# Kernel optimization log

Hardware: AMD Instinct MI355X
Metric: run time of the kernel (lower is better)

## Reference

```python
import jax, jax.numpy as jnp
import numpy as np

B, T, E, DH = 4, 4096, 1024, 128

def setup_inputs() -> dict:
    key = jax.random.key(0)
    k1, k2, k3, k4 = jax.random.split(key, 4)
    scale = 1.0 / np.sqrt(E)
    return {
        "norm_inputs": jax.random.normal(k1, (B, T, E), dtype=jnp.float32),
        "Wq": jax.random.normal(k2, (E, DH), dtype=jnp.float32) * scale,
        "Wk": jax.random.normal(k3, (E, DH), dtype=jnp.float32) * scale,
        "Wv": jax.random.normal(k4, (E, DH), dtype=jnp.float32) * scale,
    }

def reference(norm_inputs, Wq, Wk, Wv):
    # q,k,v: [B,T,DH]
    q = jnp.einsum("bte,ed->btd", norm_inputs, Wq)
    k = jnp.einsum("bte,ed->btd", norm_inputs, Wk)
    v = jnp.einsum("bte,ed->btd", norm_inputs, Wv)
    Tn = norm_inputs.shape[1]
    # scaled scores [B,T,T]
    scores = jnp.einsum("bqd,bkd->bqk", q, k) / jnp.sqrt(jnp.asarray(q.shape[-1], q.dtype))
    causal = jnp.tril(jnp.ones((Tn, Tn), dtype=bool))
    scores = jnp.where(causal, scores, -jnp.inf)
    attn = jax.nn.softmax(scores, axis=-1)  # dropout p=0 -> identity
    return jnp.einsum("bqk,bkd->bqd", attn, v)
```

## Files before the change

### kernel.cpp

```cpp
#include <hip/hip_runtime.h>
#include <hip/hip_bf16.h>

#define NB 4
#define NT 4096
#define NE 1024
#define ND 128
#define QSCALE 0.12751741f

typedef unsigned u32x4 __attribute__((ext_vector_type(4)));
typedef float f32x4 __attribute__((ext_vector_type(4)));
typedef float f32x16 __attribute__((ext_vector_type(16)));
typedef __bf16 bf16x8 __attribute__((ext_vector_type(8)));
typedef unsigned short u16;

__device__ __forceinline__ unsigned cvt_pk_bf16(float lo, float hi) {
  unsigned r;
  asm("v_cvt_pk_bf16_f32 %0, %1, %2" : "=v"(r) : "v"(lo), "v"(hi));
  return r;
}
__device__ __forceinline__ void permswap(unsigned& a, unsigned& b) {
  asm("v_permlane32_swap_b32 %0, %1" : "+v"(a), "+v"(b));
}
__device__ __forceinline__ u16 f2bf(float f) {
  unsigned x = __float_as_uint(f);
  x += 0x7fffu + ((x >> 16) & 1u);
  return (u16)(x >> 16);
}
__device__ __forceinline__ f32x16 mfma32(bf16x8 a, bf16x8 b, f32x16 c) {
  return __builtin_amdgcn_mfma_f32_32x32x16_bf16(a, b, c, 0, 0, 0);
}
__device__ __forceinline__ bf16x8 ldb(const u16* p) {
  return *reinterpret_cast<const bf16x8*>(p);
}
__device__ __forceinline__ void pack_pf(const f32x16& pr, bf16x8& f0, bf16x8& f1) {
  unsigned pk[8];
#pragma unroll
  for (int i = 0; i < 8; ++i) pk[i] = cvt_pk_bf16(pr[2 * i], pr[2 * i + 1]);
  permswap(pk[0], pk[2]);
  permswap(pk[1], pk[3]);
  permswap(pk[4], pk[6]);
  permswap(pk[5], pk[7]);
  u32x4 t0, t1;
  t0[0] = pk[0]; t0[1] = pk[1]; t0[2] = pk[2]; t0[3] = pk[3];
  t1[0] = pk[4]; t1[1] = pk[5]; t1[2] = pk[6]; t1[3] = pk[7];
  f0 = __builtin_bit_cast(bf16x8, t0);
  f1 = __builtin_bit_cast(bf16x8, t1);
}

__global__ void ah_prep(const float* __restrict__ Wq, const float* __restrict__ Wk,
                        const float* __restrict__ Wv, u16* __restrict__ wt) {
  const int m = blockIdx.x >> 5;
  const int r = blockIdx.x & 31;
  const int e0 = (r >> 1) * 64;
  const int d0 = (r & 1) * 64;
  const float* W = (m == 0) ? Wq : (m == 1) ? Wk : Wv;
  const float s = (m == 0) ? QSCALE : 1.0f;
  __shared__ u16 lds[64][68];
  const int t = threadIdx.x;
  const int row = t >> 2;
  const int c0 = (t & 3) * 16;
  const float* src = W + (size_t)(e0 + row) * ND + d0 + c0;
#pragma unroll
  for (int i = 0; i < 16; i += 4) {
    f32x4 v = *reinterpret_cast<const f32x4*>(src + i);
#pragma unroll
    for (int j = 0; j < 4; ++j) lds[c0 + i + j][row] = f2bf(v[j] * s);
  }
  __syncthreads();
  const int d = t >> 2;
  const int ec = (t & 3) * 16;
  u16* dst = wt + (size_t)m * NE * ND + (size_t)(d0 + d) * NE + e0 + ec;
  u32x4 o0, o1;
#pragma unroll
  for (int j = 0; j < 4; ++j)
    o0[j] = (unsigned)lds[d][ec + 2 * j] | ((unsigned)lds[d][ec + 2 * j + 1] << 16);
#pragma unroll
  for (int j = 0; j < 4; ++j)
    o1[j] = (unsigned)lds[d][ec + 8 + 2 * j] | ((unsigned)lds[d][ec + 8 + 2 * j + 1] << 16);
  *reinterpret_cast<u32x4*>(dst) = o0;
  *reinterpret_cast<u32x4*>(dst + 8) = o1;
}

__global__ __launch_bounds__(256, 2) void ah_proj(
    const float* __restrict__ X, const u16* __restrict__ wt,
    u16* __restrict__ qb, u16* __restrict__ kb, u16* __restrict__ vtb) {
  const int row0 = blockIdx.x * 32;
  const int tid = threadIdx.x;
  const int w = tid >> 6;
  const int lane = tid & 63;
  const int l31 = lane & 31;
  const int h = lane >> 5;

  const float* xrow = X + (size_t)(row0 + l31) * NE + h * 8;
  const u16* wpQ = wt + (size_t)(w * 32 + l31) * NE + h * 8;
  const u16* wpK = wpQ + (size_t)NE * ND;
  const u16* wpV = wpK + (size_t)NE * ND;

  f32x16 accQ = {}, accK = {}, accV = {};

#pragma unroll 2
  for (int e0 = 0; e0 < NE; e0 += 16) {
    f32x4 x0 = *reinterpret_cast<const f32x4*>(xrow + e0);
    f32x4 x1 = *reinterpret_cast<const f32x4*>(xrow + e0 + 4);
    u32x4 xw;
    xw[0] = cvt_pk_bf16(x0[0], x0[1]);
    xw[1] = cvt_pk_bf16(x0[2], x0[3]);
    xw[2] = cvt_pk_bf16(x1[0], x1[1]);
    xw[3] = cvt_pk_bf16(x1[2], x1[3]);
    bf16x8 xf = __builtin_bit_cast(bf16x8, xw);
    accQ = mfma32(xf, ldb(wpQ + e0), accQ);
    accK = mfma32(xf, ldb(wpK + e0), accK);
    accV = mfma32(ldb(wpV + e0), xf, accV);
  }

  const int col = w * 32 + l31;
#pragma unroll
  for (int r = 0; r < 16; ++r) {
    const int trow = row0 + (r & 3) + 8 * (r >> 2) + 4 * h;
    qb[(size_t)trow * ND + col] = f2bf(accQ[r]);
    kb[(size_t)trow * ND + col] = f2bf(accK[r]);
  }
  const int bb = row0 >> 12;
  const int tt = (row0 & 4095) + l31;
#pragma unroll
  for (int r = 0; r < 16; ++r) {
    const int d = w * 32 + (r & 3) + 8 * (r >> 2) + 4 * h;
    vtb[(size_t)bb * ND * NT + (size_t)d * NT + tt] = f2bf(accV[r]);
  }
}

__global__ __launch_bounds__(256, 2) void ah_attn(
    const u16* __restrict__ qg, const u16* __restrict__ kg,
    const u16* __restrict__ vtg, float* __restrict__ out) {
  __shared__ float smem_m[4][32];
  __shared__ float smem_l[4][32];
  __shared__ float smem_linv[32];
  __shared__ float smemO[128][33];

  const int bid = blockIdx.x;
  const int xcd = bid & 7;
  const int slot = bid >> 3;
  const int b = xcd >> 1;
  const int qt = 127 - (slot * 2 + (xcd & 1));
  const int q0 = qt * 32;
  const int tid = threadIdx.x;
  const int w = tid >> 6;
  const int lane = tid & 63;
  const int l31 = lane & 31;
  const int h = lane >> 5;

  const u16* Qb = qg + (size_t)b * NT * ND;
  const u16* Kb = kg + (size_t)b * NT * ND;
  const u16* VTb = vtg + (size_t)b * ND * NT;
  float* Ob = out + (size_t)b * NT * ND;

  bf16x8 qf[8];
  {
    const u16* qrow = Qb + (size_t)(q0 + l31) * ND + h * 8;
#pragma unroll
    for (int s = 0; s < 8; ++s) qf[s] = ldb(qrow + s * 16);
  }

  float m_run = -1e30f, l_run = 0.f;
  f32x16 ot[4] = {};

  const int ntiles = qt + 1;
  for (int j0 = w; j0 < ntiles; j0 += 8) {
    const int j1 = j0 + 4;
    const bool has1 = (j1 < ntiles);
    const int k0 = j0 * 32;
    const int k1 = has1 ? j1 * 32 : k0;
    f32x16 sa = {}, sb = {};
    const u16* krow0 = Kb + (size_t)(k0 + l31) * ND + h * 8;
    const u16* krow1 = Kb + (size_t)(k1 + l31) * ND + h * 8;
#pragma unroll
    for (int s = 0; s < 8; ++s) {
      sa = mfma32(ldb(krow0 + s * 16), qf[s], sa);
      sb = mfma32(ldb(krow1 + s * 16), qf[s], sb);
    }
    if (j0 == qt) {
#pragma unroll
      for (int r = 0; r < 16; ++r) {
        const int kk = (r & 3) + 8 * (r >> 2) + 4 * h;
        if (kk > l31) sa[r] = -1e30f;
      }
    }
    if (has1) {
      if (j1 == qt) {
#pragma unroll
        for (int r = 0; r < 16; ++r) {
          const int kk = (r & 3) + 8 * (r >> 2) + 4 * h;
          if (kk > l31) sb[r] = -1e30f;
        }
      }
    } else {
#pragma unroll
      for (int r = 0; r < 16; ++r) sb[r] = -1e30f;
    }
    float mt = sa[0];
#pragma unroll
    for (int r = 1; r < 16; ++r) mt = fmaxf(mt, sa[r]);
#pragma unroll
    for (int r = 0; r < 16; ++r) mt = fmaxf(mt, sb[r]);
    mt = fmaxf(mt, __shfl_xor(mt, 32));
    if (__any(mt > m_run + 8.f)) {
      const float mn = fmaxf(m_run, mt);
      const float f = __builtin_amdgcn_exp2f(m_run - mn);
      l_run *= f;
#pragma unroll
      for (int d0 = 0; d0 < 4; ++d0) ot[d0] *= f;
      m_run = mn;
    }
    float ps = 0.f;
#pragma unroll
    for (int r = 0; r < 16; ++r) {
      sa[r] = __builtin_amdgcn_exp2f(sa[r] - m_run);
      ps += sa[r];
    }
#pragma unroll
    for (int r = 0; r < 16; ++r) {
      sb[r] = __builtin_amdgcn_exp2f(sb[r] - m_run);
      ps += sb[r];
    }
    ps += __shfl_xor(ps, 32);
    l_run += ps;
    bf16x8 pf0a, pf0b, pf1a, pf1b;
    pack_pf(sa, pf0a, pf0b);
    pack_pf(sb, pf1a, pf1b);
#pragma unroll
    for (int d0 = 0; d0 < 4; ++d0) {
      const u16* vrow0 = VTb + (size_t)(d0 * 32 + l31) * NT + k0 + h * 8;
      const u16* vrow1 = VTb + (size_t)(d0 * 32 + l31) * NT + k1 + h * 8;
      ot[d0] = mfma32(ldb(vrow0), pf0a, ot[d0]);
      ot[d0] = mfma32(ldb(vrow0 + 16), pf0b, ot[d0]);
      ot[d0] = mfma32(ldb(vrow1), pf1a, ot[d0]);
      ot[d0] = mfma32(ldb(vrow1 + 16), pf1b, ot[d0]);
    }
  }

  if (h == 0) { smem_m[w][l31] = m_run; smem_l[w][l31] = l_run; }
  __syncthreads();
  float mstar = smem_m[0][l31];
#pragma unroll
  for (int wv = 1; wv < 4; ++wv) mstar = fmaxf(mstar, smem_m[wv][l31]);
  float lstar = 0.f;
#pragma unroll
  for (int wv = 0; wv < 4; ++wv)
    lstar += smem_l[wv][l31] * __builtin_amdgcn_exp2f(smem_m[wv][l31] - mstar);
  if (tid < 32) smem_linv[tid] = 1.0f / lstar;
  const float fw = __builtin_amdgcn_exp2f(m_run - mstar);
  for (int rnd = 0; rnd < 4; ++rnd) {
    if (w == rnd) {
#pragma unroll
      for (int d0 = 0; d0 < 4; ++d0)
#pragma unroll
        for (int r = 0; r < 16; ++r) {
          const int d = d0 * 32 + (r & 3) + 8 * (r >> 2) + 4 * h;
          const float v = ot[d0][r] * fw;
          if (rnd == 0) smemO[d][l31] = v;
          else smemO[d][l31] += v;
        }
    }
    __syncthreads();
  }
  {
    const int q = tid >> 3;
    const int dbase = (tid & 7) * 16;
    const float linv = smem_linv[q];
    float* orow = Ob + (size_t)(q0 + q) * ND + dbase;
#pragma unroll
    for (int c = 0; c < 4; ++c) {
      f32x4 v4;
#pragma unroll
      for (int e = 0; e < 4; ++e) v4[e] = smemO[dbase + c * 4 + e][q] * linv;
      *reinterpret_cast<f32x4*>(orow + c * 4) = v4;
    }
  }
}

extern "C" void kernel_launch(void* const* d_in, const int* in_sizes, int n_in,
                              void* d_out, int out_size, void* d_ws, size_t ws_size,
                              hipStream_t stream) {
  const float* X = (const float*)d_in[0];
  const float* Wq = (const float*)d_in[1];
  const float* Wk = (const float*)d_in[2];
  const float* Wv = (const float*)d_in[3];
  u16* ws = (u16*)d_ws;
  u16* wt = ws;
  u16* qb = wt + 393216;
  u16* kb = qb + 2097152;
  u16* vtb = kb + 2097152;
  float* out = (float*)d_out;

  ah_prep<<<96, 256, 0, stream>>>(Wq, Wk, Wv, wt);
  ah_proj<<<512, 256, 0, stream>>>(X, wt, qb, kb, vtb);
  ah_attn<<<512, 256, 0, stream>>>(qb, kb, vtb, out);
}
```

Before: 265.2 us.

## Split causal attention along the key axis into chunks and add a combine kernel

```diff
diff --git a/kernel.cpp b/kernel.cpp
--- a/kernel.cpp
+++ b/kernel.cpp
@@ -25,6 +25,9 @@
   unsigned x = __float_as_uint(f);
   x += 0x7fffu + ((x >> 16) & 1u);
   return (u16)(x >> 16);
+}
+__device__ __forceinline__ float bf2f(u16 u) {
+  return __uint_as_float(((unsigned)u) << 16);
 }
 __device__ __forceinline__ f32x16 mfma32(bf16x8 a, bf16x8 b, f32x16 c) {
   return __builtin_amdgcn_mfma_f32_32x32x16_bf16(a, b, c, 0, 0, 0);
@@ -98,7 +101,7 @@
 
   f32x16 accQ = {}, accK = {}, accV = {};
 
-#pragma unroll 2
+#pragma unroll 4
   for (int e0 = 0; e0 < NE; e0 += 16) {
     f32x4 x0 = *reinterpret_cast<const f32x4*>(xrow + e0);
     f32x4 x1 = *reinterpret_cast<const f32x4*>(xrow + e0 + 4);
@@ -129,20 +132,29 @@
   }
 }
 
-__global__ __launch_bounds__(256, 2) void ah_attn(
+__global__ __launch_bounds__(256, 4) void ah_attn_sk(
     const u16* __restrict__ qg, const u16* __restrict__ kg,
-    const u16* __restrict__ vtg, float* __restrict__ out) {
+    const u16* __restrict__ vtg, u16* __restrict__ opart,
+    float* __restrict__ ml) {
   __shared__ float smem_m[4][32];
   __shared__ float smem_l[4][32];
-  __shared__ float smem_linv[32];
   __shared__ float smemO[128][33];
 
   const int bid = blockIdx.x;
-  const int xcd = bid & 7;
-  const int slot = bid >> 3;
-  const int b = xcd >> 1;
-  const int qt = 127 - (slot * 2 + (xcd & 1));
+  const int x = bid & 7;
+  const int s = bid >> 3;
+  const int b = x >> 1;
+  const int p = x & 1;
+  int r, c;
+  if (s < 64)       { r = s >> 2;               c = s & 3; }
+  else if (s < 112) { int t = s - 64; int q3 = t / 3; r = 16 + q3; c = t - 3 * q3; }
+  else if (s < 144) { int t = s - 112; r = 32 + (t >> 1); c = t & 1; }
+  else              { r = 48 + (s - 144);       c = 0; }
+  const int qt = (126 + p) - 2 * r;
   const int q0 = qt * 32;
+  const int jbeg = c * 32;
+  const int jend = min(jbeg + 32, qt + 1);
+
   const int tid = threadIdx.x;
   const int w = tid >> 6;
   const int lane = tid & 63;
@@ -152,56 +164,54 @@
   const u16* Qb = qg + (size_t)b * NT * ND;
   const u16* Kb = kg + (size_t)b * NT * ND;
   const u16* VTb = vtg + (size_t)b * ND * NT;
-  float* Ob = out + (size_t)b * NT * ND;
 
   bf16x8 qf[8];
   {
     const u16* qrow = Qb + (size_t)(q0 + l31) * ND + h * 8;
 #pragma unroll
-    for (int s = 0; s < 8; ++s) qf[s] = ldb(qrow + s * 16);
+    for (int sI = 0; sI < 8; ++sI) qf[sI] = ldb(qrow + sI * 16);
   }
 
   float m_run = -1e30f, l_run = 0.f;
   f32x16 ot[4] = {};
 
-  const int ntiles = qt + 1;
-  for (int j0 = w; j0 < ntiles; j0 += 8) {
+  for (int j0 = jbeg + w; j0 < jend; j0 += 8) {
     const int j1 = j0 + 4;
-    const bool has1 = (j1 < ntiles);
+    const bool has1 = (j1 < jend);
     const int k0 = j0 * 32;
     const int k1 = has1 ? j1 * 32 : k0;
     f32x16 sa = {}, sb = {};
     const u16* krow0 = Kb + (size_t)(k0 + l31) * ND + h * 8;
     const u16* krow1 = Kb + (size_t)(k1 + l31) * ND + h * 8;
 #pragma unroll
-    for (int s = 0; s < 8; ++s) {
-      sa = mfma32(ldb(krow0 + s * 16), qf[s], sa);
-      sb = mfma32(ldb(krow1 + s * 16), qf[s], sb);
+    for (int sI = 0; sI < 8; ++sI) {
+      sa = mfma32(ldb(krow0 + sI * 16), qf[sI], sa);
+      sb = mfma32(ldb(krow1 + sI * 16), qf[sI], sb);
     }
     if (j0 == qt) {
 #pragma unroll
-      for (int r = 0; r < 16; ++r) {
-        const int kk = (r & 3) + 8 * (r >> 2) + 4 * h;
-        if (kk > l31) sa[r] = -1e30f;
+      for (int r2 = 0; r2 < 16; ++r2) {
+        const int kk = (r2 & 3) + 8 * (r2 >> 2) + 4 * h;
+        if (kk > l31) sa[r2] = -1e30f;
       }
     }
     if (has1) {
       if (j1 == qt) {
 #pragma unroll
-        for (int r = 0; r < 16; ++r) {
-          const int kk = (r & 3) + 8 * (r >> 2) + 4 * h;
-          if (kk > l31) sb[r] = -1e30f;
+        for (int r2 = 0; r2 < 16; ++r2) {
+          const int kk = (r2 & 3) + 8 * (r2 >> 2) + 4 * h;
+          if (kk > l31) sb[r2] = -1e30f;
         }
       }
     } else {
 #pragma unroll
-      for (int r = 0; r < 16; ++r) sb[r] = -1e30f;
+      for (int r2 = 0; r2 < 16; ++r2) sb[r2] = -1e30f;
     }
     float mt = sa[0];
 #pragma unroll
-    for (int r = 1; r < 16; ++r) mt = fmaxf(mt, sa[r]);
-#pragma unroll
-    for (int r = 0; r < 16; ++r) mt = fmaxf(mt, sb[r]);
+    for (int r2 = 1; r2 < 16; ++r2) mt = fmaxf(mt, sa[r2]);
+#pragma unroll
+    for (int r2 = 0; r2 < 16; ++r2) mt = fmaxf(mt, sb[r2]);
     mt = fmaxf(mt, __shfl_xor(mt, 32));
     if (__any(mt > m_run + 8.f)) {
       const float mn = fmaxf(m_run, mt);
@@ -213,14 +223,14 @@
     }
     float ps = 0.f;
 #pragma unroll
-    for (int r = 0; r < 16; ++r) {
-      sa[r] = __builtin_amdgcn_exp2f(sa[r] - m_run);
-      ps += sa[r];
-    }
-#pragma unroll
-    for (int r = 0; r < 16; ++r) {
-      sb[r] = __builtin_amdgcn_exp2f(sb[r] - m_run);
-      ps += sb[r];
+    for (int r2 = 0; r2 < 16; ++r2) {
+      sa[r2] = __builtin_amdgcn_exp2f(sa[r2] - m_run);
+      ps += sa[r2];
+    }
+#pragma unroll
+    for (int r2 = 0; r2 < 16; ++r2) {
+      sb[r2] = __builtin_amdgcn_exp2f(sb[r2] - m_run);
+      ps += sb[r2];
     }
     ps += __shfl_xor(ps, 32);
     l_run += ps;
@@ -247,34 +257,101 @@
 #pragma unroll
   for (int wv = 0; wv < 4; ++wv)
     lstar += smem_l[wv][l31] * __builtin_amdgcn_exp2f(smem_m[wv][l31] - mstar);
-  if (tid < 32) smem_linv[tid] = 1.0f / lstar;
   const float fw = __builtin_amdgcn_exp2f(m_run - mstar);
   for (int rnd = 0; rnd < 4; ++rnd) {
     if (w == rnd) {
 #pragma unroll
       for (int d0 = 0; d0 < 4; ++d0)
 #pragma unroll
-        for (int r = 0; r < 16; ++r) {
-          const int d = d0 * 32 + (r & 3) + 8 * (r >> 2) + 4 * h;
-          const float v = ot[d0][r] * fw;
+        for (int r2 = 0; r2 < 16; ++r2) {
+          const int d = d0 * 32 + (r2 & 3) + 8 * (r2 >> 2) + 4 * h;
+          const float v = ot[d0][r2] * fw;
           if (rnd == 0) smemO[d][l31] = v;
           else smemO[d][l31] += v;
         }
     }
     __syncthreads();
   }
+  const int slot = ((b * 128 + qt) << 2) + c;
+  if (tid < 32) {
+    ml[(size_t)slot * 64 + tid] = mstar;
+    ml[(size_t)slot * 64 + 32 + tid] = lstar;
+  }
   {
     const int q = tid >> 3;
     const int dbase = (tid & 7) * 16;
-    const float linv = smem_linv[q];
-    float* orow = Ob + (size_t)(q0 + q) * ND + dbase;
-#pragma unroll
-    for (int c = 0; c < 4; ++c) {
-      f32x4 v4;
-#pragma unroll
-      for (int e = 0; e < 4; ++e) v4[e] = smemO[dbase + c * 4 + e][q] * linv;
-      *reinterpret_cast<f32x4*>(orow + c * 4) = v4;
-    }
+    u32x4 o0, o1;
+#pragma unroll
+    for (int k = 0; k < 4; ++k)
+      o0[k] = cvt_pk_bf16(smemO[dbase + 2 * k][q], smemO[dbase + 2 * k + 1][q]);
+#pragma unroll
+    for (int k = 0; k < 4; ++k)
+      o1[k] = cvt_pk_bf16(smemO[dbase + 8 + 2 * k][q], smemO[dbase + 9 + 2 * k][q]);
+    u16* dst = opart + (size_t)slot * 4096 + q * ND + dbase;
+    *reinterpret_cast<u32x4*>(dst) = o0;
+    *reinterpret_cast<u32x4*>(dst + 8) = o1;
+  }
+}
+
+__global__ __launch_bounds__(256, 4) void ah_comb(
+    const u16* __restrict__ opart, const float* __restrict__ ml,
+    float* __restrict__ out) {
+  const int bid = blockIdx.x;
+  const int x = bid & 7;
+  const int r = bid >> 3;
+  const int b = x >> 1;
+  const int p = x & 1;
+  const int qt = (126 + p) - 2 * r;
+  const int q0 = qt * 32;
+  const int nch = (qt + 32) >> 5;
+  const int slot0 = (b * 128 + qt) << 2;
+
+  const int tid = threadIdx.x;
+  const int q = tid >> 3;
+  const int dbase = (tid & 7) * 16;
+
+  float mi0 = -1e30f, mi1 = -1e30f, mi2 = -1e30f, mi3 = -1e30f;
+  mi0 = ml[(size_t)slot0 * 64 + q];
+  if (nch > 1) mi1 = ml[(size_t)(slot0 + 1) * 64 + q];
+  if (nch > 2) mi2 = ml[(size_t)(slot0 + 2) * 64 + q];
+  if (nch > 3) mi3 = ml[(size_t)(slot0 + 3) * 64 + q];
+  const float M = fmaxf(fmaxf(mi0, mi1), fmaxf(mi2, mi3));
+  float sc0 = __builtin_amdgcn_exp2f(mi0 - M);
+  float sc1 = __builtin_amdgcn_exp2f(mi1 - M);
+  float sc2 = __builtin_amdgcn_exp2f(mi2 - M);
+  float sc3 = __builtin_amdgcn_exp2f(mi3 - M);
+  float L = ml[(size_t)slot0 * 64 + 32 + q] * sc0;
+  if (nch > 1) L += ml[(size_t)(slot0 + 1) * 64 + 32 + q] * sc1;
+  if (nch > 2) L += ml[(size_t)(slot0 + 2) * 64 + 32 + q] * sc2;
+  if (nch > 3) L += ml[(size_t)(slot0 + 3) * 64 + 32 + q] * sc3;
+
+  float acc[16];
+#pragma unroll
+  for (int k = 0; k < 16; ++k) acc[k] = 0.f;
+#pragma unroll
+  for (int i = 0; i < 4; ++i) {
+    if (i < nch) {
+      const float sc = (i == 0) ? sc0 : (i == 1) ? sc1 : (i == 2) ? sc2 : sc3;
+      const u16* src = opart + (size_t)(slot0 + i) * 4096 + q * ND + dbase;
+      u32x4 w0 = *reinterpret_cast<const u32x4*>(src);
+      u32x4 w1 = *reinterpret_cast<const u32x4*>(src + 8);
+#pragma unroll
+      for (int k = 0; k < 4; ++k) {
+        acc[2 * k] += sc * __uint_as_float(w0[k] << 16);
+        acc[2 * k + 1] += sc * __uint_as_float(w0[k] & 0xffff0000u);
+        acc[8 + 2 * k] += sc * __uint_as_float(w1[k] << 16);
+        acc[9 + 2 * k] += sc * __uint_as_float(w1[k] & 0xffff0000u);
+      }
+    }
+  }
+  const float linv = 1.0f / L;
+  float* orow = out + (size_t)b * NT * ND + (size_t)(q0 + q) * ND + dbase;
+#pragma unroll
+  for (int cc = 0; cc < 4; ++cc) {
+    f32x4 v4;
+#pragma unroll
+    for (int e = 0; e < 4; ++e) v4[e] = acc[cc * 4 + e] * linv;
+    *reinterpret_cast<f32x4*>(orow + cc * 4) = v4;
   }
 }
 
@@ -290,9 +367,12 @@
   u16* qb = wt + 393216;
   u16* kb = qb + 2097152;
   u16* vtb = kb + 2097152;
+  u16* opart = vtb + 2097152;
+  float* ml = (float*)(opart + 8388608);
   float* out = (float*)d_out;
 
   ah_prep<<<96, 256, 0, stream>>>(Wq, Wk, Wv, wt);
   ah_proj<<<512, 256, 0, stream>>>(X, wt, qb, kb, vtb);
-  ah_attn<<<512, 256, 0, stream>>>(qb, kb, vtb, out);
-}
+  ah_attn_sk<<<1280, 256, 0, stream>>>(qb, kb, vtb, opart, ml);
+  ah_comb<<<512, 256, 0, stream>>>(opart, ml, out);
+}
```

Measured after the change: 312.0 us. 17.6% more time.
